# Performance work log

Measured on AMD Instinct MI355X. Metric: run time of the kernel, lower is better.

## Reference

```python
import jax, jax.numpy as jnp
import numpy as np

N, E, F_IN, H, L, E_FEAT, G, OUT = 100000, 1600000, 8, 128, 4, 16, 256, 256


def setup_inputs() -> dict:
    key = jax.random.key(0)
    ks = jax.random.split(key, 12)
    inp = {
        "x": jax.random.normal(ks[0], (N, F_IN), jnp.float32),
        "edge_index": jax.random.randint(ks[1], (2, E), 0, N),
        "edge_attr": jax.random.uniform(ks[2], (E, E_FEAT), jnp.float32),
        "batch": jnp.sort(jax.random.randint(ks[3], (N,), 0, G)),
        "emb_W": jax.random.normal(ks[4], (F_IN, H), jnp.float32) / np.sqrt(F_IN),
        "emb_b": jnp.zeros((H,), jnp.float32),
        "edge_W": jax.random.normal(ks[5], (L, E_FEAT, H), jnp.float32) / np.sqrt(E_FEAT),
        "edge_b": jnp.zeros((L, H), jnp.float32),
        "nn_W": jax.random.normal(ks[6], (L, H, H), jnp.float32) / np.sqrt(H),
        "nn_b": jnp.zeros((L, H), jnp.float32),
        "bn_g": jnp.ones((L, H), jnp.float32),
        "bn_b": jnp.zeros((L, H), jnp.float32),
        "lin_W": jax.random.normal(ks[7], (H, OUT), jnp.float32) / np.sqrt(H),
        "lin_b": jnp.zeros((OUT,), jnp.float32),
    }
    return inp


def reference(x, edge_index, edge_attr, batch, emb_W, emb_b, edge_W, edge_b,
              nn_W, nn_b, bn_g, bn_b, lin_W, lin_b):
    eps_bn = 1e-5
    src, dst = edge_index[0], edge_index[1]
    h = x @ emb_W + emb_b  # node embedding [N,H]
    for l in range(L):
        e = edge_attr @ edge_W[l] + edge_b[l]          # [E,H] edge embedding
        msg = jax.nn.relu(h[src] + e)                   # gather + message
        agg = jax.ops.segment_sum(msg, dst, num_segments=N)  # scatter-add
        hc = (h + agg) @ nn_W[l] + nn_b[l]             # GINE nn (eps=0)
        mu = jnp.mean(hc, axis=0)
        var = jnp.mean((hc - mu) ** 2, axis=0)          # biased var (train BN)
        hc = (hc - mu) * jax.lax.rsqrt(var + eps_bn) * bn_g[l] + bn_b[l]
        hc = jax.nn.gelu(hc, approximate=False)
        h = h + hc                                      # 'res' residual
    out = h @ lin_W + lin_b                             # [N,OUT]
    rep = jax.ops.segment_sum(out, batch, num_segments=G)  # global_add_pool
    return rep
```

## Files before the change

### kernel.cpp

```cpp
#include <hip/hip_runtime.h>
#include <hip/hip_fp16.h>
#include <math.h>

#define GG 256

typedef __attribute__((ext_vector_type(8))) short short8;
typedef __attribute__((ext_vector_type(4))) float f32x4;

__device__ __forceinline__ unsigned short f2bf(float x) {
  union { float f; unsigned u; } v; v.f = x;
  unsigned r = v.u + 0x7fff + ((v.u >> 16) & 1);
  return (unsigned short)(r >> 16);
}

__device__ __forceinline__ unsigned pack_h2(float a, float b) {
  __half2 h = __floats2half2_rn(a, b);
  return *(unsigned*)&h;
}

__global__ __launch_bounds__(256) void k_emb(const float* __restrict__ x,
    const float* __restrict__ W, const float* __restrict__ b,
    float* __restrict__ h, unsigned short* __restrict__ hb, int N) {
  int idx = blockIdx.x * 256 + threadIdx.x;
  if (idx >= N * 32) return;
  int n = idx >> 5, q = idx & 31;
  const float* xr = x + (size_t)n * 8;
  float xs[8];
#pragma unroll
  for (int k = 0; k < 8; ++k) xs[k] = xr[k];
  float4 acc = ((const float4*)b)[q];
#pragma unroll
  for (int k = 0; k < 8; ++k) {
    float4 w = ((const float4*)(W + (size_t)k * 128))[q];
    acc.x += xs[k] * w.x; acc.y += xs[k] * w.y;
    acc.z += xs[k] * w.z; acc.w += xs[k] * w.w;
  }
  ((float4*)h)[idx] = acc;
  ushort4 hv4 = make_ushort4(f2bf(acc.x), f2bf(acc.y), f2bf(acc.z), f2bf(acc.w));
  *(ushort4*)(hb + (size_t)idx * 4) = hv4;
}

__global__ __launch_bounds__(256) void k_wconv(const float* __restrict__ eW,
    unsigned* __restrict__ eW16) {
  int i = blockIdx.x * 256 + threadIdx.x;
  if (i >= 4096) return;
  float2 wp = *(const float2*)(eW + (size_t)i * 2);
  eW16[i] = pack_h2(wp.x, wp.y);
}

__global__ __launch_bounds__(256) void k_nnconv(const float* __restrict__ W,
    unsigned short* __restrict__ WT) {
  int i = blockIdx.x * 256 + threadIdx.x;
  if (i >= 4 * 128 * 128) return;
  int n = i & 127, k = (i >> 7) & 127, l = i >> 14;
  WT[((size_t)(l * 128 + n)) * 128 + k] = f2bf(W[i]);
}

__global__ void k_hist(const int* __restrict__ dst, int* __restrict__ deg, int E) {
  int e = blockIdx.x * blockDim.x + threadIdx.x;
  if (e < E) atomicAdd(&deg[dst[e]], 1);
}

__global__ __launch_bounds__(256) void k_scan_reduce(const int* __restrict__ deg,
    int* __restrict__ bsum, int N) {
  __shared__ int sd[256];
  int i = blockIdx.x * 256 + threadIdx.x;
  sd[threadIdx.x] = (i < N) ? deg[i] : 0;
  __syncthreads();
  for (int s = 128; s > 0; s >>= 1) {
    if (threadIdx.x < s) sd[threadIdx.x] += sd[threadIdx.x + s];
    __syncthreads();
  }
  if (threadIdx.x == 0) bsum[blockIdx.x] = sd[0];
}

__global__ __launch_bounds__(512) void k_scan_mid(int* bsum, int nb) {
  __shared__ int sd[512];
  int t = threadIdx.x;
  int v = (t < nb) ? bsum[t] : 0;
  sd[t] = v; __syncthreads();
  for (int d = 1; d < 512; d <<= 1) {
    int xv = (t >= d) ? sd[t - d] : 0;
    __syncthreads();
    sd[t] += xv;
    __syncthreads();
  }
  if (t < nb) bsum[t] = sd[t] - v;
}

__global__ __launch_bounds__(256) void k_scan_final(const int* __restrict__ deg,
    const int* __restrict__ bsum, int* __restrict__ offs,
    int* __restrict__ cursor, int N) {
  __shared__ int sd[256];
  int t = threadIdx.x;
  int i = blockIdx.x * 256 + t;
  int v = (i < N) ? deg[i] : 0;
  sd[t] = v; __syncthreads();
  for (int d = 1; d < 256; d <<= 1) {
    int xv = (t >= d) ? sd[t - d] : 0;
    __syncthreads();
    sd[t] += xv;
    __syncthreads();
  }
  int off = bsum[blockIdx.x] + sd[t] - v;
  if (i < N) {
    offs[i] = off; cursor[i] = off;
    if (i == N - 1) offs[N] = off + v;
  }
}

__global__ void k_fill(const int* __restrict__ src, const int* __restrict__ dst,
    const float* __restrict__ attr, int* __restrict__ cursor,
    int* __restrict__ csrc, uint4* __restrict__ cattr16, int E) {
  int e = blockIdx.x * blockDim.x + threadIdx.x;
  if (e >= E) return;
  int d = dst[e];
  int pos = atomicAdd(&cursor[d], 1);
  csrc[pos] = src[e];
  const float4* a = (const float4*)(attr + (size_t)e * 16);
  float4 a0 = a[0], a1 = a[1], a2 = a[2], a3 = a[3];
  uint4 o0, o1;
  o0.x = pack_h2(a0.x, a0.y); o0.y = pack_h2(a0.z, a0.w);
  o0.z = pack_h2(a1.x, a1.y); o0.w = pack_h2(a1.z, a1.w);
  o1.x = pack_h2(a2.x, a2.y); o1.y = pack_h2(a2.z, a2.w);
  o1.z = pack_h2(a3.x, a3.y); o1.w = pack_h2(a3.z, a3.w);
  cattr16[(size_t)pos * 2] = o0;
  cattr16[(size_t)pos * 2 + 1] = o1;
}

__global__ void k_gstart(const int* __restrict__ batch, int* __restrict__ gstart,
                         int N, int Gn) {
  int i = blockIdx.x * blockDim.x + threadIdx.x;
  if (i >= N) return;
  int b = batch[i];
  if (i == 0) { for (int g = 0; g <= b; ++g) gstart[g] = 0; }
  else { int bp = batch[i - 1]; for (int g = bp + 1; g <= b; ++g) gstart[g] = i; }
  if (i == N - 1) { for (int g = b + 1; g <= Gn; ++g) gstart[g] = N; }
}

__global__ __launch_bounds__(256) void k_edge_agg(const float* __restrict__ h,
    const unsigned* __restrict__ hb32,
    const uint4* __restrict__ cattr16, const int* __restrict__ csrc,
    const int* __restrict__ offs, const unsigned* __restrict__ eW16,
    const float* __restrict__ eb, unsigned* __restrict__ hpa16,
    float* __restrict__ cstats, int N) {
  int t = threadIdx.x;
  if (blockIdx.x == 0) cstats[t] = 0.f;
  int n = blockIdx.x * 4 + (t >> 6);
  if (n >= N) return;
  int l = t & 63;
  __half2 w2[16];
#pragma unroll
  for (int k = 0; k < 16; ++k) {
    unsigned u = eW16[k * 64 + l];
    w2[k] = *(__half2*)&u;
  }
  float2 bias = *(const float2*)(eb + 2 * l);
  const unsigned* hb_l = hb32 + l;
  int jb = offs[n], je = offs[n + 1];
  jb = __builtin_amdgcn_readfirstlane(jb);
  je = __builtin_amdgcn_readfirstlane(je);

#define EDGE(JJ, ACC)                                                       \
  {                                                                         \
    int s = csrc[(JJ)];                                                     \
    uint4 p0 = cattr16[(size_t)(JJ) * 2];                                   \
    uint4 p1 = cattr16[(size_t)(JJ) * 2 + 1];                               \
    unsigned u = hb_l[(size_t)s * 64];                                      \
    __half2 ev = __floats2half2_rn(0.f, 0.f);                               \
    const unsigned pw[8] = {p0.x, p0.y, p0.z, p0.w, p1.x, p1.y, p1.z, p1.w};\
    _Pragma("unroll")                                                       \
    for (int k = 0; k < 8; ++k) {                                           \
      __half2 ap = *(__half2*)&pw[k];                                       \
      ev = __hfma2(__half2half2(__low2half(ap)), w2[2 * k], ev);            \
      ev = __hfma2(__half2half2(__high2half(ap)), w2[2 * k + 1], ev);       \
    }                                                                       \
    float e0 = __low2float(ev), e1 = __high2float(ev);                      \
    union { unsigned uu; float ff; } c0, c1;                                \
    c0.uu = u << 16; c1.uu = u & 0xffff0000u;                               \
    ACC.x += fmaxf(e0 + bias.x + c0.ff, 0.f);                               \
    ACC.y += fmaxf(e1 + bias.y + c1.ff, 0.f);                               \
  }

  float2 a0 = make_float2(0.f, 0.f), a1 = a0, a2 = a0, a3 = a0;
  float2 a4 = a0, a5 = a0, a6 = a0, a7 = a0;
  int j = jb;
  for (; j + 8 <= je; j += 8) {
    EDGE(j, a0) EDGE(j + 1, a1) EDGE(j + 2, a2) EDGE(j + 3, a3)
    EDGE(j + 4, a4) EDGE(j + 5, a5) EDGE(j + 6, a6) EDGE(j + 7, a7)
  }
  if (j + 4 <= je) {
    EDGE(j, a0) EDGE(j + 1, a1) EDGE(j + 2, a2) EDGE(j + 3, a3)
    j += 4;
  }
  for (; j < je; ++j) EDGE(j, a0)
#undef EDGE
  float2 hvv = *(const float2*)(h + (size_t)n * 128 + 2 * l);
  float rx = hvv.x + (((a0.x + a1.x) + (a2.x + a3.x)) + ((a4.x + a5.x) + (a6.x + a7.x)));
  float ry = hvv.y + (((a0.y + a1.y) + (a2.y + a3.y)) + ((a4.y + a5.y) + (a6.y + a7.y)));
  hpa16[(size_t)n * 64 + l] = ((unsigned)f2bf(ry) << 16) | (unsigned)f2bf(rx);
}

__global__ __launch_bounds__(256) void k_gemm_mfma(
    const unsigned short* __restrict__ A16, const unsigned short* __restrict__ WT16,
    const float* __restrict__ bias, float* __restrict__ hc,
    float* __restrict__ cstats, int N) {
  __shared__ short a_lds[128 * 136];
  __shared__ short w_lds[128 * 136];
  int t = threadIdx.x;
  int rowbase = blockIdx.x * 128;
  {
    int r = t >> 1;
    int off = (t & 1) * 64;
    const short* ga = (const short*)A16 + (size_t)(rowbase + r) * 128 + off;
    short* la = &a_lds[r * 136 + off];
    const short* gw = (const short*)WT16 + (size_t)r * 128 + off;
    short* lw = &w_lds[r * 136 + off];
    if (rowbase + r < N) {
#pragma unroll
      for (int jj = 0; jj < 8; ++jj)
        *(uint4*)(la + jj * 8) = *(const uint4*)(ga + jj * 8);
    } else {
#pragma unroll
      for (int jj = 0; jj < 8; ++jj)
        *(uint4*)(la + jj * 8) = make_uint4(0, 0, 0, 0);
    }
#pragma unroll
    for (int jj = 0; jj < 8; ++jj)
      *(uint4*)(lw + jj * 8) = *(const uint4*)(gw + jj * 8);
  }
  __syncthreads();
  int w = t >> 6;
  int lane = t & 63;
  int l15 = lane & 15, quad = lane >> 4;
  f32x4 acc[2][8];
#pragma unroll
  for (int rt = 0; rt < 2; ++rt)
#pragma unroll
    for (int nt = 0; nt < 8; ++nt)
      acc[rt][nt] = (f32x4){0.f, 0.f, 0.f, 0.f};
#pragma unroll
  for (int kc = 0; kc < 4; ++kc) {
    int k0 = kc * 32 + quad * 8;
    short8 af0 = *(const short8*)&a_lds[(w * 32 + l15) * 136 + k0];
    short8 af1 = *(const short8*)&a_lds[(w * 32 + 16 + l15) * 136 + k0];
#pragma unroll
    for (int nt = 0; nt < 8; ++nt) {
      short8 bf = *(const short8*)&w_lds[(nt * 16 + l15) * 136 + k0];
      acc[0][nt] = __builtin_amdgcn_mfma_f32_16x16x32_bf16(af0, bf, acc[0][nt], 0, 0, 0);
      acc[1][nt] = __builtin_amdgcn_mfma_f32_16x16x32_bf16(af1, bf, acc[1][nt], 0, 0, 0);
    }
  }
  float sA[8], sQ[8];
#pragma unroll
  for (int nt = 0; nt < 8; ++nt) { sA[nt] = 0.f; sQ[nt] = 0.f; }
#pragma unroll
  for (int nt = 0; nt < 8; ++nt) {
    int col = nt * 16 + l15;
    float bv = bias[col];
#pragma unroll
    for (int rt = 0; rt < 2; ++rt) {
      int rbase = rowbase + w * 32 + rt * 16 + quad * 4;
#pragma unroll
      for (int reg = 0; reg < 4; ++reg) {
        int row = rbase + reg;
        float v = acc[rt][nt][reg] + bv;
        if (row < N) {
          hc[(size_t)row * 128 + col] = v;
          sA[nt] += v; sQ[nt] += v * v;
        }
      }
    }
  }
#pragma unroll
  for (int nt = 0; nt < 8; ++nt) {
    sA[nt] += __shfl_xor(sA[nt], 16);
    sA[nt] += __shfl_xor(sA[nt], 32);
    sQ[nt] += __shfl_xor(sQ[nt], 16);
    sQ[nt] += __shfl_xor(sQ[nt], 32);
  }
  __syncthreads();
  float* sdA = (float*)a_lds;
  float* sdQ = (float*)w_lds;
  if (quad == 0) {
#pragma unroll
    for (int nt = 0; nt < 8; ++nt) {
      sdA[w * 128 + nt * 16 + l15] = sA[nt];
      sdQ[w * 128 + nt * 16 + l15] = sQ[nt];
    }
  }
  __syncthreads();
  if (t < 128) {
    float s = sdA[t] + sdA[128 + t] + sdA[256 + t] + sdA[384 + t];
    float s2 = sdQ[t] + sdQ[128 + t] + sdQ[256 + t] + sdQ[384 + t];
    atomicAdd(&cstats[t], s);
    atomicAdd(&cstats[128 + t], s2);
  }
}

__global__ __launch_bounds__(256) void k_bn(const float* __restrict__ hc,
    const float* __restrict__ cstats,
    const float* __restrict__ g, const float* __restrict__ bb,
    float* __restrict__ h, unsigned short* __restrict__ hb, int N) {
  int idx = blockIdx.x * 256 + threadIdx.x;
  if (idx >= N * 32) return;
  int q = idx & 31;
  float invN = 1.f / (float)N;
  float4 cs = ((const float4*)cstats)[q];
  float4 cq = ((const float4*)cstats)[q + 32];
  float4 gv = ((const float4*)g)[q];
  float4 bv = ((const float4*)bb)[q];
  float4 v = ((const float4*)hc)[idx];
  float4 hv = ((const float4*)h)[idx];
#define BN1(X)                                                      \
  { float mu = cs.X * invN;                                         \
    float var = cq.X * invN - mu * mu;                              \
    float xn = (v.X - mu) * rsqrtf(var + 1e-5f) * gv.X + bv.X;      \
    hv.X += 0.5f * xn * (1.f + erff(xn * 0.70710678118654752f)); }
  BN1(x) BN1(y) BN1(z) BN1(w)
#undef BN1
  ((float4*)h)[idx] = hv;
  if (hb) {
    ushort4 hv4 = make_ushort4(f2bf(hv.x), f2bf(hv.y), f2bf(hv.z), f2bf(hv.w));
    *(ushort4*)(hb + (size_t)idx * 4) = hv4;
  }
}

__global__ __launch_bounds__(256) void k_poolfinal(const float* __restrict__ h,
    const int* __restrict__ gstart, const float* __restrict__ W,
    const float* __restrict__ b, float* __restrict__ out) {
  int g = blockIdx.x;
  int t = threadIdx.x, c = t & 127, half = t >> 7;
  int n0 = gstart[g], n1 = gstart[g + 1];
  float s = 0.f;
  for (int n = n0 + half; n < n1; n += 2) s += h[(size_t)n * 128 + c];
  __shared__ float ls[256];
  __shared__ float pr[128];
  ls[t] = s; __syncthreads();
  if (t < 128) pr[t] = ls[t] + ls[t + 128];
  __syncthreads();
  float cnt = (float)(n1 - n0);
  float acc = cnt * b[t];
#pragma unroll 8
  for (int k = 0; k < 128; ++k) acc += pr[k] * W[(size_t)k * 256 + t];
  out[(size_t)g * 256 + t] = acc;
}

extern "C" void kernel_launch(void* const* d_in, const int* in_sizes, int n_in,
                              void* d_out, int out_size, void* d_ws, size_t ws_size,
                              hipStream_t stream) {
  const float* x     = (const float*)d_in[0];
  const int*   eidx  = (const int*)d_in[1];
  const float* eattr = (const float*)d_in[2];
  const int*   batch = (const int*)d_in[3];
  const float* embW  = (const float*)d_in[4];
  const float* embB  = (const float*)d_in[5];
  const float* edgeW = (const float*)d_in[6];
  const float* edgeB = (const float*)d_in[7];
  const float* nnW   = (const float*)d_in[8];
  const float* nnB   = (const float*)d_in[9];
  const float* bnG   = (const float*)d_in[10];
  const float* bnB   = (const float*)d_in[11];
  const float* linW  = (const float*)d_in[12];
  const float* linB  = (const float*)d_in[13];
  float* out = (float*)d_out;

  int N = in_sizes[0] / 8;
  int E = in_sizes[1] / 2;
  const int* src = eidx;
  const int* dst = eidx + E;

  char* wptr = (char*)d_ws;
  auto alloc = [&](size_t bytes) {
    char* p = wptr; wptr += (bytes + 255) & ~(size_t)255; return p;
  };
  float* h      = (float*)alloc((size_t)N * 128 * 4);
  float* hc     = (float*)alloc((size_t)N * 128 * 4);
  unsigned short* hb = (unsigned short*)alloc((size_t)N * 128 * 2);
  unsigned* hpa16 = (unsigned*)alloc((size_t)N * 64 * 4);
  uint4* cattr16 = (uint4*)alloc((size_t)E * 32);
  int*   csrc   = (int*)alloc((size_t)E * 4);
  int*   offs   = (int*)alloc((size_t)(N + 1) * 4);
  int*   cursor = (int*)alloc((size_t)N * 4);
  int*   deg    = (int*)alloc((size_t)N * 4);
  int nb = (N + 255) / 256;
  int*   bsum   = (int*)alloc((size_t)nb * 4);
  float* cstats = (float*)alloc(256 * 4);
  unsigned* eW16 = (unsigned*)alloc(4096 * 4);
  unsigned short* WT16 = (unsigned short*)alloc(4 * 128 * 128 * 2);
  int*   gstart = (int*)alloc((size_t)(GG + 1) * 4);

  int q32 = (N * 32 + 255) / 256;

  hipMemsetAsync(deg, 0, (size_t)N * 4, stream);
  k_emb<<<q32, 256, 0, stream>>>(x, embW, embB, h, hb, N);
  k_wconv<<<16, 256, 0, stream>>>(edgeW, eW16);
  k_nnconv<<<256, 256, 0, stream>>>(nnW, WT16);
  k_hist<<<(E + 255) / 256, 256, 0, stream>>>(dst, deg, E);
  k_scan_reduce<<<nb, 256, 0, stream>>>(deg, bsum, N);
  k_scan_mid<<<1, 512, 0, stream>>>(bsum, nb);
  k_scan_final<<<nb, 256, 0, stream>>>(deg, bsum, offs, cursor, N);
  k_fill<<<(E + 255) / 256, 256, 0, stream>>>(src, dst, eattr, cursor, csrc, cattr16, E);
  k_gstart<<<(N + 255) / 256, 256, 0, stream>>>(batch, gstart, N, GG);

  int gblk = (N + 127) / 128;
  for (int l = 0; l < 4; ++l) {
    k_edge_agg<<<(N + 3) / 4, 256, 0, stream>>>(h, (const unsigned*)hb, cattr16, csrc,
        offs, eW16 + (size_t)l * 1024, edgeB + (size_t)l * 128, hpa16, cstats, N);
    k_gemm_mfma<<<gblk, 256, 0, stream>>>((const unsigned short*)hpa16,
        WT16 + (size_t)l * 128 * 128, nnB + (size_t)l * 128, hc, cstats, N);
    k_bn<<<q32, 256, 0, stream>>>(hc, cstats,
        bnG + (size_t)l * 128, bnB + (size_t)l * 128, h, (l == 3) ? nullptr : hb, N);
  }
  k_poolfinal<<<GG, 256, 0, stream>>>(h, gstart, linW, linB, out);
}
```

Before: 1.206 ms.

## Use fdot2 for edge embedding, persistent grid-stride edge aggregation, batched gathers

Edge-weight packing now pairs consecutive input features per output channel, so the edge embedding can be computed with v_dot2 fp16 dot products that accumulate in fp32. This replaces the previous half2 broadcast-FMA chain that accumulated in fp16. The aggregation kernel becomes persistent: 2048 blocks grid-stride over nodes, so weight loads are amortised across many nodes, and source indices and h gathers are issued eight at a time ahead of the math to overlap latency. Accumulators drop from eight to two per lane, which may lengthen dependency chains, and fp32 accumulation slightly changes numerics.

New measurement: 1.141 ms. 5.4% less time.

```diff
diff --git a/kernel.cpp b/kernel.cpp
--- a/kernel.cpp
+++ b/kernel.cpp
@@ -6,6 +6,7 @@
 
 typedef __attribute__((ext_vector_type(8))) short short8;
 typedef __attribute__((ext_vector_type(4))) float f32x4;
+typedef _Float16 half2v __attribute__((ext_vector_type(2)));
 
 __device__ __forceinline__ unsigned short f2bf(float x) {
   union { float f; unsigned u; } v; v.f = x;
@@ -16,6 +17,13 @@
 __device__ __forceinline__ unsigned pack_h2(float a, float b) {
   __half2 h = __floats2half2_rn(a, b);
   return *(unsigned*)&h;
+}
+
+__device__ __forceinline__ float fdot2u(unsigned a, unsigned b, float c) {
+  half2v av, bv;
+  __builtin_memcpy(&av, &a, 4);
+  __builtin_memcpy(&bv, &b, 4);
+  return __builtin_amdgcn_fdot2(av, bv, c, false);
 }
 
 __global__ __launch_bounds__(256) void k_emb(const float* __restrict__ x,
@@ -41,11 +49,12 @@
 }
 
 __global__ __launch_bounds__(256) void k_wconv(const float* __restrict__ eW,
-    unsigned* __restrict__ eW16) {
+    unsigned* __restrict__ eWp) {
   int i = blockIdx.x * 256 + threadIdx.x;
   if (i >= 4096) return;
-  float2 wp = *(const float2*)(eW + (size_t)i * 2);
-  eW16[i] = pack_h2(wp.x, wp.y);
+  int c = i & 127, k = (i >> 7) & 7, l = i >> 10;
+  const float* base = eW + ((size_t)(l * 16 + 2 * k) * 128 + c);
+  eWp[i] = pack_h2(base[0], base[128]);
 }
 
 __global__ __launch_bounds__(256) void k_nnconv(const float* __restrict__ W,
@@ -141,64 +150,76 @@
 __global__ __launch_bounds__(256) void k_edge_agg(const float* __restrict__ h,
     const unsigned* __restrict__ hb32,
     const uint4* __restrict__ cattr16, const int* __restrict__ csrc,
-    const int* __restrict__ offs, const unsigned* __restrict__ eW16,
+    const int* __restrict__ offs, const unsigned* __restrict__ eWp,
     const float* __restrict__ eb, unsigned* __restrict__ hpa16,
     float* __restrict__ cstats, int N) {
   int t = threadIdx.x;
   if (blockIdx.x == 0) cstats[t] = 0.f;
-  int n = blockIdx.x * 4 + (t >> 6);
-  if (n >= N) return;
   int l = t & 63;
-  __half2 w2[16];
-#pragma unroll
-  for (int k = 0; k < 16; ++k) {
-    unsigned u = eW16[k * 64 + l];
-    w2[k] = *(__half2*)&u;
-  }
+  int wid = blockIdx.x * 4 + (t >> 6);
+  int nw = gridDim.x * 4;
+  uint2 wp[8];
+#pragma unroll
+  for (int k = 0; k < 8; ++k) wp[k] = *(const uint2*)&eWp[k * 128 + 2 * l];
   float2 bias = *(const float2*)(eb + 2 * l);
   const unsigned* hb_l = hb32 + l;
-  int jb = offs[n], je = offs[n + 1];
-  jb = __builtin_amdgcn_readfirstlane(jb);
-  je = __builtin_amdgcn_readfirstlane(je);
-
-#define EDGE(JJ, ACC)                                                       \
+
+#define EDGE2(JJ, UU, AX, AY)                                               \
   {                                                                         \
-    int s = csrc[(JJ)];                                                     \
-    uint4 p0 = cattr16[(size_t)(JJ) * 2];                                   \
-    uint4 p1 = cattr16[(size_t)(JJ) * 2 + 1];                               \
-    unsigned u = hb_l[(size_t)s * 64];                                      \
-    __half2 ev = __floats2half2_rn(0.f, 0.f);                               \
-    const unsigned pw[8] = {p0.x, p0.y, p0.z, p0.w, p1.x, p1.y, p1.z, p1.w};\
-    _Pragma("unroll")                                                       \
-    for (int k = 0; k < 8; ++k) {                                           \
-      __half2 ap = *(__half2*)&pw[k];                                       \
-      ev = __hfma2(__half2half2(__low2half(ap)), w2[2 * k], ev);            \
-      ev = __hfma2(__half2half2(__high2half(ap)), w2[2 * k + 1], ev);       \
-    }                                                                       \
-    float e0 = __low2float(ev), e1 = __high2float(ev);                      \
+    uint4 q0 = cattr16[(size_t)(JJ) * 2];                                   \
+    uint4 q1 = cattr16[(size_t)(JJ) * 2 + 1];                               \
+    float e0 = bias.x, e1 = bias.y;                                         \
+    e0 = fdot2u(q0.x, wp[0].x, e0); e1 = fdot2u(q0.x, wp[0].y, e1);         \
+    e0 = fdot2u(q0.y, wp[1].x, e0); e1 = fdot2u(q0.y, wp[1].y, e1);         \
+    e0 = fdot2u(q0.z, wp[2].x, e0); e1 = fdot2u(q0.z, wp[2].y, e1);         \
+    e0 = fdot2u(q0.w, wp[3].x, e0); e1 = fdot2u(q0.w, wp[3].y, e1);         \
+    e0 = fdot2u(q1.x, wp[4].x, e0); e1 = fdot2u(q1.x, wp[4].y, e1);         \
+    e0 = fdot2u(q1.y, wp[5].x, e0); e1 = fdot2u(q1.y, wp[5].y, e1);         \
+    e0 = fdot2u(q1.z, wp[6].x, e0); e1 = fdot2u(q1.z, wp[6].y, e1);         \
+    e0 = fdot2u(q1.w, wp[7].x, e0); e1 = fdot2u(q1.w, wp[7].y, e1);         \
     union { unsigned uu; float ff; } c0, c1;                                \
-    c0.uu = u << 16; c1.uu = u & 0xffff0000u;                               \
-    ACC.x += fmaxf(e0 + bias.x + c0.ff, 0.f);                               \
-    ACC.y += fmaxf(e1 + bias.y + c1.ff, 0.f);                               \
-  }
-
-  float2 a0 = make_float2(0.f, 0.f), a1 = a0, a2 = a0, a3 = a0;
-  float2 a4 = a0, a5 = a0, a6 = a0, a7 = a0;
-  int j = jb;
-  for (; j + 8 <= je; j += 8) {
-    EDGE(j, a0) EDGE(j + 1, a1) EDGE(j + 2, a2) EDGE(j + 3, a3)
-    EDGE(j + 4, a4) EDGE(j + 5, a5) EDGE(j + 6, a6) EDGE(j + 7, a7)
-  }
-  if (j + 4 <= je) {
-    EDGE(j, a0) EDGE(j + 1, a1) EDGE(j + 2, a2) EDGE(j + 3, a3)
-    j += 4;
-  }
-  for (; j < je; ++j) EDGE(j, a0)
-#undef EDGE
-  float2 hvv = *(const float2*)(h + (size_t)n * 128 + 2 * l);
-  float rx = hvv.x + (((a0.x + a1.x) + (a2.x + a3.x)) + ((a4.x + a5.x) + (a6.x + a7.x)));
-  float ry = hvv.y + (((a0.y + a1.y) + (a2.y + a3.y)) + ((a4.y + a5.y) + (a6.y + a7.y)));
-  hpa16[(size_t)n * 64 + l] = ((unsigned)f2bf(ry) << 16) | (unsigned)f2bf(rx);
+    c0.uu = (UU) << 16; c1.uu = (UU) & 0xffff0000u;                         \
+    AX += fmaxf(e0 + c0.ff, 0.f);                                           \
+    AY += fmaxf(e1 + c1.ff, 0.f);                                           \
+  }
+
+  for (int n = wid; n < N; n += nw) {
+    int jb = offs[n], je = offs[n + 1];
+    jb = __builtin_amdgcn_readfirstlane(jb);
+    je = __builtin_amdgcn_readfirstlane(je);
+    float ax = 0.f, ay = 0.f, bx = 0.f, by = 0.f;
+    int j = jb;
+    for (; j + 8 <= je; j += 8) {
+      int s0 = csrc[j + 0], s1 = csrc[j + 1], s2 = csrc[j + 2], s3 = csrc[j + 3];
+      int s4 = csrc[j + 4], s5 = csrc[j + 5], s6 = csrc[j + 6], s7 = csrc[j + 7];
+      unsigned u0 = hb_l[(size_t)s0 * 64], u1 = hb_l[(size_t)s1 * 64];
+      unsigned u2 = hb_l[(size_t)s2 * 64], u3 = hb_l[(size_t)s3 * 64];
+      unsigned u4 = hb_l[(size_t)s4 * 64], u5 = hb_l[(size_t)s5 * 64];
+      unsigned u6 = hb_l[(size_t)s6 * 64], u7 = hb_l[(size_t)s7 * 64];
+      EDGE2(j + 0, u0, ax, ay) EDGE2(j + 1, u1, bx, by)
+      EDGE2(j + 2, u2, ax, ay) EDGE2(j + 3, u3, bx, by)
+      EDGE2(j + 4, u4, ax, ay) EDGE2(j + 5, u5, bx, by)
+      EDGE2(j + 6, u6, ax, ay) EDGE2(j + 7, u7, bx, by)
+    }
+    if (j + 4 <= je) {
+      int s0 = csrc[j + 0], s1 = csrc[j + 1], s2 = csrc[j + 2], s3 = csrc[j + 3];
+      unsigned u0 = hb_l[(size_t)s0 * 64], u1 = hb_l[(size_t)s1 * 64];
+      unsigned u2 = hb_l[(size_t)s2 * 64], u3 = hb_l[(size_t)s3 * 64];
+      EDGE2(j + 0, u0, ax, ay) EDGE2(j + 1, u1, bx, by)
+      EDGE2(j + 2, u2, ax, ay) EDGE2(j + 3, u3, bx, by)
+      j += 4;
+    }
+    for (; j < je; ++j) {
+      int s0 = csrc[j];
+      unsigned u0 = hb_l[(size_t)s0 * 64];
+      EDGE2(j, u0, ax, ay)
+    }
+    float2 hvv = *(const float2*)(h + (size_t)n * 128 + 2 * l);
+    float rx = hvv.x + ax + bx;
+    float ry = hvv.y + ay + by;
+    hpa16[(size_t)n * 64 + l] = ((unsigned)f2bf(ry) << 16) | (unsigned)f2bf(rx);
+  }
+#undef EDGE2
 }
 
 __global__ __launch_bounds__(256) void k_gemm_mfma(
@@ -405,7 +426,7 @@
 
   int gblk = (N + 127) / 128;
   for (int l = 0; l < 4; ++l) {
-    k_edge_agg<<<(N + 3) / 4, 256, 0, stream>>>(h, (const unsigned*)hb, cattr16, csrc,
+    k_edge_agg<<<2048, 256, 0, stream>>>(h, (const unsigned*)hb, cattr16, csrc,
         offs, eW16 + (size_t)l * 1024, edgeB + (size_t)l * 128, hpa16, cstats, N);
     k_gemm_mfma<<<gblk, 256, 0, stream>>>((const unsigned short*)hpa16,
         WT16 + (size_t)l * 128 * 128, nnB + (size_t)l * 128, hc, cstats, N);
```

## Compute edge embeddings with MFMA in edge aggregation, scalar-load source indices

Applied to the files above, without the earlier changes.

The per-edge 16x128 edge-attribute projection moves from packed half2 FMAs per lane to MFMA 16x16x16 f16 tiles over 16 edges at a time. Results are staged through per-wave LDS before the gather/ReLU/accumulate epilogue. Source indices are fetched with scalar s_load_dwordx8 and the kernel becomes a grid-stride persistent loop over nodes, with edge weights pre-laid out in MFMA B-fragment order. This trades ALU-heavy half FMAs for matrix cores, at the cost of LDS round-trips, wasted tile slots for low-degree nodes, and over-reads past the edge arrays covered by padding.

New measurement: 1.064 ms. -11.7%, faster.

```diff
diff --git a/kernel.cpp b/kernel.cpp
--- a/kernel.cpp
+++ b/kernel.cpp
@@ -6,6 +6,8 @@
 
 typedef __attribute__((ext_vector_type(8))) short short8;
 typedef __attribute__((ext_vector_type(4))) float f32x4;
+typedef _Float16 half4v __attribute__((ext_vector_type(4)));
+typedef __attribute__((ext_vector_type(8))) unsigned uint8v;
 
 __device__ __forceinline__ unsigned short f2bf(float x) {
   union { float f; unsigned u; } v; v.f = x;
@@ -16,6 +18,17 @@
 __device__ __forceinline__ unsigned pack_h2(float a, float b) {
   __half2 h = __floats2half2_rn(a, b);
   return *(unsigned*)&h;
+}
+
+__device__ __forceinline__ uint8v sload8(const void* p) {
+  uint8v r;
+  asm volatile("s_load_dwordx8 %0, %1, 0x0"
+               : "=s"(r) : "s"((unsigned long long)p));
+  return r;
+}
+__device__ __forceinline__ void swait() {
+  asm volatile("s_waitcnt lgkmcnt(0)" ::: "memory");
+  __builtin_amdgcn_sched_barrier(0);
 }
 
 __global__ __launch_bounds__(256) void k_emb(const float* __restrict__ x,
@@ -40,12 +53,17 @@
   *(ushort4*)(hb + (size_t)idx * 4) = hv4;
 }
 
-__global__ __launch_bounds__(256) void k_wconv(const float* __restrict__ eW,
-    unsigned* __restrict__ eW16) {
+__global__ __launch_bounds__(256) void k_wconv2(const float* __restrict__ eW,
+    unsigned* __restrict__ eWf) {
   int i = blockIdx.x * 256 + threadIdx.x;
-  if (i >= 4096) return;
-  float2 wp = *(const float2*)(eW + (size_t)i * 2);
-  eW16[i] = pack_h2(wp.x, wp.y);
+  if (i >= 2048) return;
+  int lane = i & 63, nt = (i >> 6) & 7, l = i >> 9;
+  int l15 = lane & 15, quad = lane >> 4;
+  const float* base = eW + (size_t)l * 16 * 128 + (size_t)(nt * 16 + l15);
+  unsigned lo = pack_h2(base[(quad * 4 + 0) * 128], base[(quad * 4 + 1) * 128]);
+  unsigned hi = pack_h2(base[(quad * 4 + 2) * 128], base[(quad * 4 + 3) * 128]);
+  eWf[(size_t)i * 2] = lo;
+  eWf[(size_t)i * 2 + 1] = hi;
 }
 
 __global__ __launch_bounds__(256) void k_nnconv(const float* __restrict__ W,
@@ -141,64 +159,81 @@
 __global__ __launch_bounds__(256) void k_edge_agg(const float* __restrict__ h,
     const unsigned* __restrict__ hb32,
     const uint4* __restrict__ cattr16, const int* __restrict__ csrc,
-    const int* __restrict__ offs, const unsigned* __restrict__ eW16,
+    const int* __restrict__ offs, const unsigned* __restrict__ eWf,
     const float* __restrict__ eb, unsigned* __restrict__ hpa16,
     float* __restrict__ cstats, int N) {
+  __shared__ float elds_all[4][16 * 132];
   int t = threadIdx.x;
   if (blockIdx.x == 0) cstats[t] = 0.f;
-  int n = blockIdx.x * 4 + (t >> 6);
-  if (n >= N) return;
-  int l = t & 63;
-  __half2 w2[16];
-#pragma unroll
-  for (int k = 0; k < 16; ++k) {
-    unsigned u = eW16[k * 64 + l];
-    w2[k] = *(__half2*)&u;
-  }
-  float2 bias = *(const float2*)(eb + 2 * l);
-  const unsigned* hb_l = hb32 + l;
-  int jb = offs[n], je = offs[n + 1];
-  jb = __builtin_amdgcn_readfirstlane(jb);
-  je = __builtin_amdgcn_readfirstlane(je);
-
-#define EDGE(JJ, ACC)                                                       \
-  {                                                                         \
-    int s = csrc[(JJ)];                                                     \
-    uint4 p0 = cattr16[(size_t)(JJ) * 2];                                   \
-    uint4 p1 = cattr16[(size_t)(JJ) * 2 + 1];                               \
-    unsigned u = hb_l[(size_t)s * 64];                                      \
-    __half2 ev = __floats2half2_rn(0.f, 0.f);                               \
-    const unsigned pw[8] = {p0.x, p0.y, p0.z, p0.w, p1.x, p1.y, p1.z, p1.w};\
-    _Pragma("unroll")                                                       \
-    for (int k = 0; k < 8; ++k) {                                           \
-      __half2 ap = *(__half2*)&pw[k];                                       \
-      ev = __hfma2(__half2half2(__low2half(ap)), w2[2 * k], ev);            \
-      ev = __hfma2(__half2half2(__high2half(ap)), w2[2 * k + 1], ev);       \
-    }                                                                       \
-    float e0 = __low2float(ev), e1 = __high2float(ev);                      \
+  int lane = t & 63;
+  int l15 = lane & 15, quad = lane >> 4;
+  int wid = blockIdx.x * 4 + (t >> 6);
+  int nw = gridDim.x * 4;
+  float* elds = elds_all[t >> 6];
+  uint2 bfr[8];
+#pragma unroll
+  for (int nt = 0; nt < 8; ++nt) bfr[nt] = ((const uint2*)eWf)[nt * 64 + lane];
+  float2 bias = *(const float2*)(eb + 2 * lane);
+  const unsigned* hb_l = hb32 + lane;
+
+#define GI(r, SC)                                                           \
+  unsigned u##r = 0;                                                        \
+  if (j0 + (r) < je) u##r = hb_l[(size_t)(unsigned)(SC) * 64];
+
+#define EPI(r, UU, AX, AY)                                                  \
+  if (j0 + (r) < je) {                                                      \
+    float2 ev = *(const float2*)&elds[(r) * 132 + 2 * lane];                \
     union { unsigned uu; float ff; } c0, c1;                                \
-    c0.uu = u << 16; c1.uu = u & 0xffff0000u;                               \
-    ACC.x += fmaxf(e0 + bias.x + c0.ff, 0.f);                               \
-    ACC.y += fmaxf(e1 + bias.y + c1.ff, 0.f);                               \
-  }
-
-  float2 a0 = make_float2(0.f, 0.f), a1 = a0, a2 = a0, a3 = a0;
-  float2 a4 = a0, a5 = a0, a6 = a0, a7 = a0;
-  int j = jb;
-  for (; j + 8 <= je; j += 8) {
-    EDGE(j, a0) EDGE(j + 1, a1) EDGE(j + 2, a2) EDGE(j + 3, a3)
-    EDGE(j + 4, a4) EDGE(j + 5, a5) EDGE(j + 6, a6) EDGE(j + 7, a7)
-  }
-  if (j + 4 <= je) {
-    EDGE(j, a0) EDGE(j + 1, a1) EDGE(j + 2, a2) EDGE(j + 3, a3)
-    j += 4;
-  }
-  for (; j < je; ++j) EDGE(j, a0)
-#undef EDGE
-  float2 hvv = *(const float2*)(h + (size_t)n * 128 + 2 * l);
-  float rx = hvv.x + (((a0.x + a1.x) + (a2.x + a3.x)) + ((a4.x + a5.x) + (a6.x + a7.x)));
-  float ry = hvv.y + (((a0.y + a1.y) + (a2.y + a3.y)) + ((a4.y + a5.y) + (a6.y + a7.y)));
-  hpa16[(size_t)n * 64 + l] = ((unsigned)f2bf(ry) << 16) | (unsigned)f2bf(rx);
+    c0.uu = (UU) << 16; c1.uu = (UU) & 0xffff0000u;                         \
+    AX += fmaxf(ev.x + bias.x + c0.ff, 0.f);                                \
+    AY += fmaxf(ev.y + bias.y + c1.ff, 0.f);                                \
+  }
+
+  for (int n = wid; n < N; n += nw) {
+    int jb = __builtin_amdgcn_readfirstlane(offs[n]);
+    int je = __builtin_amdgcn_readfirstlane(offs[n + 1]);
+    float ax = 0.f, ay = 0.f, bx = 0.f, by = 0.f;
+    for (int j0 = jb; j0 < je; j0 += 16) {
+      uint8v scA = sload8((const char*)csrc + ((size_t)(unsigned)j0 << 2));
+      uint8v scB = sload8((const char*)csrc + ((size_t)(unsigned)(j0 + 8) << 2));
+      uint2 araw = *(const uint2*)((const char*)cattr16 +
+                    ((size_t)(unsigned)(j0 + l15)) * 32 + quad * 8);
+      swait();
+      GI(0, scA[0]) GI(1, scA[1]) GI(2, scA[2]) GI(3, scA[3])
+      GI(4, scA[4]) GI(5, scA[5]) GI(6, scA[6]) GI(7, scA[7])
+      GI(8, scB[0]) GI(9, scB[1]) GI(10, scB[2]) GI(11, scB[3])
+      GI(12, scB[4]) GI(13, scB[5]) GI(14, scB[6]) GI(15, scB[7])
+      half4v av;
+      __builtin_memcpy(&av, &araw, 8);
+      f32x4 ee[8];
+#pragma unroll
+      for (int nt = 0; nt < 8; ++nt) {
+        half4v bv;
+        __builtin_memcpy(&bv, &bfr[nt], 8);
+        ee[nt] = __builtin_amdgcn_mfma_f32_16x16x16f16(
+            av, bv, (f32x4){0.f, 0.f, 0.f, 0.f}, 0, 0, 0);
+      }
+#pragma unroll
+      for (int nt = 0; nt < 8; ++nt)
+#pragma unroll
+        for (int reg = 0; reg < 4; ++reg)
+          elds[(quad * 4 + reg) * 132 + nt * 16 + l15] = ee[nt][reg];
+      EPI(0, u0, ax, ay)  EPI(1, u1, bx, by)
+      EPI(2, u2, ax, ay)  EPI(3, u3, bx, by)
+      EPI(4, u4, ax, ay)  EPI(5, u5, bx, by)
+      EPI(6, u6, ax, ay)  EPI(7, u7, bx, by)
+      EPI(8, u8, ax, ay)  EPI(9, u9, bx, by)
+      EPI(10, u10, ax, ay) EPI(11, u11, bx, by)
+      EPI(12, u12, ax, ay) EPI(13, u13, bx, by)
+      EPI(14, u14, ax, ay) EPI(15, u15, bx, by)
+    }
+    float2 hvv = *(const float2*)(h + (size_t)n * 128 + 2 * lane);
+    float rx = hvv.x + ax + bx;
+    float ry = hvv.y + ay + by;
+    hpa16[(size_t)n * 64 + lane] = ((unsigned)f2bf(ry) << 16) | (unsigned)f2bf(rx);
+  }
+#undef GI
+#undef EPI
 }
 
 __global__ __launch_bounds__(256) void k_gemm_mfma(
@@ -378,15 +413,15 @@
   float* hc     = (float*)alloc((size_t)N * 128 * 4);
   unsigned short* hb = (unsigned short*)alloc((size_t)N * 128 * 2);
   unsigned* hpa16 = (unsigned*)alloc((size_t)N * 64 * 4);
-  uint4* cattr16 = (uint4*)alloc((size_t)E * 32);
-  int*   csrc   = (int*)alloc((size_t)E * 4);
+  uint4* cattr16 = (uint4*)alloc((size_t)E * 32 + 1024);
+  int*   csrc   = (int*)alloc((size_t)E * 4 + 256);
   int*   offs   = (int*)alloc((size_t)(N + 1) * 4);
   int*   cursor = (int*)alloc((size_t)N * 4);
   int*   deg    = (int*)alloc((size_t)N * 4);
   int nb = (N + 255) / 256;
   int*   bsum   = (int*)alloc((size_t)nb * 4);
   float* cstats = (float*)alloc(256 * 4);
-  unsigned* eW16 = (unsigned*)alloc(4096 * 4);
+  unsigned* eWf = (unsigned*)alloc(4096 * 4);
   unsigned short* WT16 = (unsigned short*)alloc(4 * 128 * 128 * 2);
   int*   gstart = (int*)alloc((size_t)(GG + 1) * 4);
 
@@ -394,7 +429,7 @@
 
   hipMemsetAsync(deg, 0, (size_t)N * 4, stream);
   k_emb<<<q32, 256, 0, stream>>>(x, embW, embB, h, hb, N);
-  k_wconv<<<16, 256, 0, stream>>>(edgeW, eW16);
+  k_wconv2<<<8, 256, 0, stream>>>(edgeW, eWf);
   k_nnconv<<<256, 256, 0, stream>>>(nnW, WT16);
   k_hist<<<(E + 255) / 256, 256, 0, stream>>>(dst, deg, E);
   k_scan_reduce<<<nb, 256, 0, stream>>>(deg, bsum, N);
@@ -405,8 +440,8 @@
 
   int gblk = (N + 127) / 128;
   for (int l = 0; l < 4; ++l) {
-    k_edge_agg<<<(N + 3) / 4, 256, 0, stream>>>(h, (const unsigned*)hb, cattr16, csrc,
-        offs, eW16 + (size_t)l * 1024, edgeB + (size_t)l * 128, hpa16, cstats, N);
+    k_edge_agg<<<8192, 256, 0, stream>>>(h, (const unsigned*)hb, cattr16, csrc,
+        offs, eWf + (size_t)l * 1024, edgeB + (size_t)l * 128, hpa16, cstats, N);
     k_gemm_mfma<<<gblk, 256, 0, stream>>>((const unsigned short*)hpa16,
         WT16 + (size_t)l * 128 * 128, nnB + (size_t)l * 128, hc, cstats, N);
     k_bn<<<q32, 256, 0, stream>>>(hc, cstats,
```
